# Optimization experiments

Measured on AMD Instinct MI355X. Metric: run time of the kernel, lower is better.

## Reference

```python
import jax, jax.numpy as jnp
import numpy as np

B, T, C = 2, 2048, 768
N_HEADS = 12
HEAD = C // N_HEADS


def setup_inputs() -> dict:
    key = jax.random.key(0)
    k1, k2, k3 = jax.random.split(key, 3)
    x = jax.random.normal(k1, (B, T, C), dtype=jnp.float32)
    # torch Linear weights: [out_features, in_features]
    W_attn = jax.random.normal(k2, (3 * C, C), dtype=jnp.float32) * 0.02
    W_proj = jax.random.normal(k3, (C, C), dtype=jnp.float32) * 0.02
    return {"x": x, "W_attn": W_attn, "W_proj": W_proj}


def reference(x, W_attn, W_proj):
    b, t, c = x.shape
    qkv = jnp.einsum('btc,oc->bto', x, W_attn)  # [B,T,3C]
    q, k, v = jnp.split(qkv, 3, axis=-1)
    # [B, H, T, D]
    q = q.reshape(b, t, N_HEADS, HEAD).transpose(0, 2, 1, 3)
    k = k.reshape(b, t, N_HEADS, HEAD).transpose(0, 2, 1, 3)
    v = v.reshape(b, t, N_HEADS, HEAD).transpose(0, 2, 1, 3)
    scale = 1.0 / jnp.sqrt(jnp.asarray(HEAD, dtype=x.dtype))
    wei = jnp.einsum('bhqd,bhkd->bhqk', q, k) * scale  # [B,H,T,T]
    causal = jnp.tril(jnp.ones((t, t), dtype=bool))
    wei = jnp.where(causal[None, None], wei, jnp.asarray(-jnp.inf, dtype=wei.dtype))
    wei = jax.nn.softmax(wei, axis=-1)  # dropout p=0 -> identity
    out = jnp.einsum('bhqk,bhkd->bhqd', wei, v)
    out = out.transpose(0, 2, 1, 3).reshape(b, t, c)
    out = jnp.einsum('btc,oc->bto', out, W_proj)
    return out
```

## Files before the change

kernel.cpp:

```cpp
#include <hip/hip_runtime.h>

#define T_DIM 2048
#define C_DIM 768
#define NH    12
#define HD    64
#define KDIM  768
#define NJOBS (24 * 32)

typedef __attribute__((ext_vector_type(8))) short short8;
typedef __attribute__((ext_vector_type(4))) float f32x4;
typedef unsigned short u16;

__device__ __forceinline__ u16 f2bf(float f) {
    unsigned int u = __builtin_bit_cast(unsigned int, f);
    u = (u + 0x7fffu + ((u >> 16) & 1u)) >> 16;
    return (u16)u;
}
__device__ __forceinline__ f32x4 max4(f32x4 a, f32x4 b) {
    f32x4 r; r[0]=fmaxf(a[0],b[0]); r[1]=fmaxf(a[1],b[1]);
    r[2]=fmaxf(a[2],b[2]); r[3]=fmaxf(a[3],b[3]); return r;
}
__device__ __forceinline__ unsigned int cvtpk(float a, float b) {
    unsigned int r;
    asm("v_cvt_pk_bf16_f32 %0, %1, %2" : "=v"(r) : "v"(a), "v"(b));
    return r;
}
__device__ __forceinline__ void gload16(const u16* g, u16* l) {
    __builtin_amdgcn_global_load_lds(
        (const __attribute__((address_space(1))) unsigned int*)g,
        (__attribute__((address_space(3))) unsigned int*)l, 16, 0, 0);
}

#define NX  (4096 * 768)
#define NWA (2304 * 768)
#define NWP (768 * 768)
#define TOT4 ((NX + NWA + NWP) / 4)

__global__ __launch_bounds__(256) void convert_all(
    const float* __restrict__ x, const float* __restrict__ wa,
    const float* __restrict__ wp, u16* __restrict__ xb,
    u16* __restrict__ wab, u16* __restrict__ wpb, int* __restrict__ counter)
{
    if (blockIdx.x == 0 && threadIdx.x == 0) *counter = 0;
    for (int i4 = blockIdx.x * 256 + threadIdx.x; i4 < TOT4; i4 += gridDim.x * 256) {
        int i = i4 * 4;
        const float* src; u16* dst; int off;
        if (i < NX)            { src = x;  dst = xb;  off = i; }
        else if (i < NX + NWA) { src = wa; dst = wab; off = i - NX; }
        else                   { src = wp; dst = wpb; off = i - NX - NWA; }
        float4 v = *(const float4*)&src[off];
        ushort4 o;
        o.x = f2bf(v.x); o.y = f2bf(v.y); o.z = f2bf(v.z); o.w = f2bf(v.w);
        *(ushort4*)&dst[off] = o;
    }
}

__global__ __launch_bounds__(256) void gemm_qkv(
    const u16* __restrict__ A, const u16* __restrict__ Wt,
    u16* __restrict__ qb, u16* __restrict__ kb, u16* __restrict__ vtb)
{
    __shared__ __align__(16) u16 AsL[2][128][32];
    __shared__ __align__(16) u16 BsL[2][128][32];

    const int tid = threadIdx.x;
    const int orig = blockIdx.x;
    const int wg = (orig & 7) * 72 + (orig >> 3);
    const int bm = (wg / 18) * 128;
    const int bn = (wg % 18) * 128;

    const int w = tid >> 6, l = tid & 63;
    const int wr = (w >> 1) * 64, wc = (w & 1) * 64;
    const int lrow = l & 15, lg = l >> 4;
    const int lr4 = l >> 2, lc4 = l & 3;

    f32x4 acc[4][4];
    const f32x4 zero4 = {0.f, 0.f, 0.f, 0.f};
#pragma unroll
    for (int mi = 0; mi < 4; ++mi)
#pragma unroll
        for (int ni = 0; ni < 4; ++ni) acc[mi][ni] = zero4;

    auto STAGE = [&](int buf, int k0) {
#pragma unroll
        for (int i = 0; i < 2; ++i) {
            const int rb = w * 32 + i * 16;
            const int row = rb + lr4;
            const int sc = (lc4 ^ (row & 3)) * 8;
            gload16(&A [(size_t)(bm + row) * KDIM + k0 + sc], &AsL[buf][rb][0]);
            gload16(&Wt[(size_t)(bn + row) * KDIM + k0 + sc], &BsL[buf][rb][0]);
        }
    };

    int cur = 0;
    STAGE(0, 0);
    for (int k0 = 0; k0 < KDIM; k0 += 32) {
        __syncthreads();
        if (k0 + 32 < KDIM) STAGE(cur ^ 1, k0 + 32);

        short8 af[4], bf[4];
#pragma unroll
        for (int mi = 0; mi < 4; ++mi)
            af[mi] = *(const short8*)&AsL[cur][wr + mi * 16 + lrow][(lg ^ (lrow & 3)) * 8];
#pragma unroll
        for (int ni = 0; ni < 4; ++ni)
            bf[ni] = *(const short8*)&BsL[cur][wc + ni * 16 + lrow][(lg ^ (lrow & 3)) * 8];
#pragma unroll
        for (int mi = 0; mi < 4; ++mi)
#pragma unroll
            for (int ni = 0; ni < 4; ++ni)
                acc[mi][ni] = __builtin_amdgcn_mfma_f32_16x16x32_bf16(
                    af[mi], bf[ni], acc[mi][ni], 0, 0, 0);
        cur ^= 1;
    }

#pragma unroll
    for (int ni = 0; ni < 4; ++ni) {
        const int colbase = bn + wc + ni * 16;
        const int which = colbase / C_DIM;
        const int h = (colbase % C_DIM) / HD;
        const int d = (colbase % HD) + lrow;
        const float qs = (which == 0) ? 0.125f : 1.0f;
#pragma unroll
        for (int mi = 0; mi < 4; ++mi) {
            const int t0 = bm + wr + mi * 16 + lg * 4;
            const int bb2 = t0 >> 11, tt = t0 & 2047;
            const size_t bhoff = (size_t)(bb2 * NH + h);
            if (which == 2) {
                ushort4 pv;
                pv.x = f2bf(acc[mi][ni][0]); pv.y = f2bf(acc[mi][ni][1]);
                pv.z = f2bf(acc[mi][ni][2]); pv.w = f2bf(acc[mi][ni][3]);
                *(ushort4*)&vtb[(bhoff * HD + d) * T_DIM + tt] = pv;
            } else {
                u16* dst = (which == 0) ? qb : kb;
#pragma unroll
                for (int jj = 0; jj < 4; ++jj)
                    dst[(bhoff * T_DIM + tt + jj) * HD + d] = f2bf(acc[mi][ni][jj] * qs);
            }
        }
    }
}

__global__ __launch_bounds__(256) void gemm_proj(
    const u16* __restrict__ A, const u16* __restrict__ Wt,
    float* __restrict__ dense)
{
    __shared__ __align__(16) u16 As[64][40];
    __shared__ __align__(16) u16 Bs[128][40];

    const int tid = threadIdx.x;
    const int orig = blockIdx.x;
    const int wg = (orig & 7) * 48 + (orig >> 3);
    const int bm = (wg / 6) * 64, bn = (wg % 6) * 128;

    const int w = tid >> 6, l = tid & 63;
    const int wr = (w >> 1) * 32, wc = (w & 1) * 64;
    const int lrow = l & 15, lg = l >> 4;

    const int srow = tid >> 2;
    const int scol = (tid & 3) * 8;

    f32x4 acc[2][4];
    const f32x4 zero4 = {0.f, 0.f, 0.f, 0.f};
#pragma unroll
    for (int mi = 0; mi < 2; ++mi)
#pragma unroll
        for (int ni = 0; ni < 4; ++ni) acc[mi][ni] = zero4;

    uint4 ra0 = *(const uint4*)&A [(size_t)(bm + srow)      * KDIM + scol];
    uint4 rb0 = *(const uint4*)&Wt[(size_t)(bn + srow)      * KDIM + scol];
    uint4 rb1 = *(const uint4*)&Wt[(size_t)(bn + 64 + srow) * KDIM + scol];

    for (int k0 = 0; k0 < KDIM; k0 += 32) {
        __syncthreads();
        *(uint4*)&As[srow][scol]      = ra0;
        *(uint4*)&Bs[srow][scol]      = rb0;
        *(uint4*)&Bs[64 + srow][scol] = rb1;
        __syncthreads();

        if (k0 + 32 < KDIM) {
            ra0 = *(const uint4*)&A [(size_t)(bm + srow)      * KDIM + k0 + 32 + scol];
            rb0 = *(const uint4*)&Wt[(size_t)(bn + srow)      * KDIM + k0 + 32 + scol];
            rb1 = *(const uint4*)&Wt[(size_t)(bn + 64 + srow) * KDIM + k0 + 32 + scol];
        }

        short8 af[2], bf[4];
#pragma unroll
        for (int mi = 0; mi < 2; ++mi)
            af[mi] = *(const short8*)&As[wr + mi * 16 + lrow][lg * 8];
#pragma unroll
        for (int ni = 0; ni < 4; ++ni)
            bf[ni] = *(const short8*)&Bs[wc + ni * 16 + lrow][lg * 8];
#pragma unroll
        for (int mi = 0; mi < 2; ++mi)
#pragma unroll
            for (int ni = 0; ni < 4; ++ni)
                acc[mi][ni] = __builtin_amdgcn_mfma_f32_16x16x32_bf16(
                    af[mi], bf[ni], acc[mi][ni], 0, 0, 0);
    }

#pragma unroll
    for (int ni = 0; ni < 4; ++ni) {
        const int col = bn + wc + ni * 16 + lrow;
#pragma unroll
        for (int mi = 0; mi < 2; ++mi) {
            const int m0 = bm + wr + mi * 16 + lg * 4;
#pragma unroll
            for (int jj = 0; jj < 4; ++jj)
                dense[(size_t)(m0 + jj) * C_DIM + col] = acc[mi][ni][jj];
        }
    }
}

__global__ __launch_bounds__(256, 2) void attn_mfma(
    const u16* __restrict__ q, const u16* __restrict__ k,
    const u16* __restrict__ vt, u16* __restrict__ aw, int* __restrict__ counter)
{
    __shared__ __align__(16) u16 KsL [2][128][64];
    __shared__ __align__(16) u16 VtsL[2][64][128];
    __shared__ __align__(16) u16 Ps  [4][16][72];
    __shared__ int job_s;

    const int tid = threadIdx.x, w = tid >> 6, l = tid & 63;
    const int lrow = l & 15, lg = l >> 4;
    const int lr8 = l >> 3, lc8 = l & 7;
    const int lr16 = l >> 4, lc16 = l & 15;
    const f32x4 zero4 = {0.f, 0.f, 0.f, 0.f};

    for (;;) {
        __syncthreads();
        if (tid == 0) job_s = atomicAdd(counter, 1);
        __syncthreads();
        const int j = job_s;
        if (j >= NJOBS) break;

        const int qt = 31 - (j / 24);
        const int bh = j - (j / 24) * 24;
        const int bb = bh / NH, hh = bh % NH;
        const int qbase = qt * 64 + w * 16;
        const int qg = qbase + lrow;

        const u16* Qp = q  + (size_t)bh * T_DIM * HD;
        const u16* Kp = k  + (size_t)bh * T_DIM * HD;
        const u16* Vp = vt + (size_t)bh * HD * T_DIM;

        const short8 aq0 = *(const short8*)&Qp[(size_t)(qbase + lrow) * HD + lg * 8];
        const short8 aq1 = *(const short8*)&Qp[(size_t)(qbase + lrow) * HD + 32 + lg * 8];

        f32x4 o[4];
#pragma unroll
        for (int n = 0; n < 4; ++n) o[n] = zero4;
        float m_run = -3.0e38f;
        float l_run = 0.0f;

        auto STAGE = [&](int buf, int kk0) {
#pragma unroll
            for (int i = 0; i < 4; ++i) {
                const int rb = w * 32 + i * 8;
                const int row = rb + lr8;
                gload16(&Kp[(size_t)(kk0 + row) * HD + ((lc8 ^ (row & 7)) * 8)],
                        &KsL[buf][rb][0]);
            }
#pragma unroll
            for (int i = 0; i < 4; ++i) {
                const int db = w * 16 + i * 4;
                const int d = db + lr16;
                gload16(&Vp[(size_t)d * T_DIM + kk0 + ((lc16 ^ (d & 15)) * 8)],
                        &VtsL[buf][db][0]);
            }
        };

        auto PROCESS = [&](f32x4* s, int sub, int kk0, bool masked) {
            if (masked) {
#pragma unroll
                for (int n = 0; n < 4; ++n)
#pragma unroll
                    for (int jj = 0; jj < 4; ++jj)
                        if (kk0 + sub * 64 + n * 16 + lg * 4 + jj > qg)
                            s[n][jj] = -3.0e38f;
            }
            f32x4 t2 = max4(max4(s[0], s[1]), max4(s[2], s[3]));
            float rm = fmaxf(fmaxf(t2[0], t2[1]), fmaxf(t2[2], t2[3]));
            rm = fmaxf(rm, __shfl_xor(rm, 16));
            rm = fmaxf(rm, __shfl_xor(rm, 32));
            const float m_new = fmaxf(m_run, rm);
            const float alpha = __expf(m_run - m_new);
            m_run = m_new;
#pragma unroll
            for (int n = 0; n < 4; ++n)
#pragma unroll
                for (int jj = 0; jj < 4; ++jj)
                    s[n][jj] = __expf(s[n][jj] - m_new);
            f32x4 a2 = (s[0] + s[1]) + (s[2] + s[3]);
            float rs = (a2[0] + a2[1]) + (a2[2] + a2[3]);
            rs += __shfl_xor(rs, 16);
            rs += __shfl_xor(rs, 32);
            l_run = l_run * alpha + rs;
#pragma unroll
            for (int n = 0; n < 4; ++n) {
                uint2 pr;
                pr.x = cvtpk(s[n][0], s[n][1]);
                pr.y = cvtpk(s[n][2], s[n][3]);
                *(uint2*)&Ps[w][lrow][n * 16 + lg * 4] = pr;
            }
#pragma unroll
            for (int jj = 0; jj < 4; ++jj) {
                const float aj = __shfl(alpha, lg * 4 + jj);
                o[0][jj] *= aj; o[1][jj] *= aj; o[2][jj] *= aj; o[3][jj] *= aj;
            }
            const short8 ap0 = *(const short8*)&Ps[w][lrow][lg * 8];
            const short8 ap1 = *(const short8*)&Ps[w][lrow][32 + lg * 8];
            const int cur = (kk0 >> 7) & 1;
#pragma unroll
            for (int n = 0; n < 4; ++n) {
                const int row = n * 16 + lrow;
                const short8 bv0 = *(const short8*)
                    &VtsL[cur][row][((sub * 8 + lg) ^ lrow) * 8];
                const short8 bv1 = *(const short8*)
                    &VtsL[cur][row][((sub * 8 + 4 + lg) ^ lrow) * 8];
                o[n] = __builtin_amdgcn_mfma_f32_16x16x32_bf16(ap0, bv0, o[n], 0, 0, 0);
                o[n] = __builtin_amdgcn_mfma_f32_16x16x32_bf16(ap1, bv1, o[n], 0, 0, 0);
            }
        };

        const int nkt = qt / 2 + 1;
        int cur = 0;
        STAGE(0, 0);
        for (int kt = 0; kt < nkt; ++kt) {
            const int kk0 = kt * 128;
            __syncthreads();
            if (kt + 1 < nkt) STAGE(cur ^ 1, kk0 + 128);

            const bool last = (kt == nkt - 1);
            const int nsub = (last && (qt & 1) == 0) ? 1 : 2;

            f32x4 s0[4], s1[4];
#pragma unroll
            for (int n = 0; n < 4; ++n) {
                const int row = n * 16 + lrow;
                const short8 kf0 = *(const short8*)&KsL[cur][row][((lg)     ^ (lrow & 7)) * 8];
                const short8 kf1 = *(const short8*)&KsL[cur][row][((lg + 4) ^ (lrow & 7)) * 8];
                s0[n] = __builtin_amdgcn_mfma_f32_16x16x32_bf16(kf0, aq0, zero4, 0, 0, 0);
                s0[n] = __builtin_amdgcn_mfma_f32_16x16x32_bf16(kf1, aq1, s0[n], 0, 0, 0);
            }
            if (nsub == 2) {
#pragma unroll
                for (int n = 0; n < 4; ++n) {
                    const int row = 64 + n * 16 + lrow;
                    const short8 kf0 = *(const short8*)&KsL[cur][row][((lg)     ^ (lrow & 7)) * 8];
                    const short8 kf1 = *(const short8*)&KsL[cur][row][((lg + 4) ^ (lrow & 7)) * 8];
                    s1[n] = __builtin_amdgcn_mfma_f32_16x16x32_bf16(kf0, aq0, zero4, 0, 0, 0);
                    s1[n] = __builtin_amdgcn_mfma_f32_16x16x32_bf16(kf1, aq1, s1[n], 0, 0, 0);
                }
            }

            PROCESS(s0, 0, kk0, last && nsub == 1);
            if (nsub == 2) PROCESS(s1, 1, kk0, last);

            cur ^= 1;
        }

#pragma unroll
        for (int jj = 0; jj < 4; ++jj) {
            const float lj = __shfl(l_run, lg * 4 + jj);
            const float inv = 1.0f / lj;
            const size_t m = (size_t)bb * T_DIM + qbase + lg * 4 + jj;
#pragma unroll
            for (int n = 0; n < 4; ++n)
                aw[m * C_DIM + hh * HD + n * 16 + lrow] = f2bf(o[n][jj] * inv);
        }
    }
}

extern "C" void kernel_launch(void* const* d_in, const int* in_sizes, int n_in,
                              void* d_out, int out_size, void* d_ws, size_t ws_size,
                              hipStream_t stream) {
    const float* x      = (const float*)d_in[0];
    const float* W_attn = (const float*)d_in[1];
    const float* W_proj = (const float*)d_in[2];
    float* out = (float*)d_out;

    char* ws = (char*)d_ws;
    u16* xb  = (u16*)ws;                       ws += (size_t)NX * 2;
    u16* wab = (u16*)ws;                       ws += (size_t)NWA * 2;
    u16* wpb = (u16*)ws;                       ws += (size_t)NWP * 2;
    u16* qb  = (u16*)ws;                       ws += (size_t)24 * T_DIM * HD * 2;
    u16* kb  = (u16*)ws;                       ws += (size_t)24 * T_DIM * HD * 2;
    u16* vtb = (u16*)ws;                       ws += (size_t)24 * T_DIM * HD * 2;
    u16* awb = (u16*)ws;                       ws += (size_t)4096 * C_DIM * 2;
    int* cnt = (int*)ws;

    convert_all<<<2048, 256, 0, stream>>>(x, W_attn, W_proj, xb, wab, wpb, cnt);

    gemm_qkv<<<576, 256, 0, stream>>>(xb, wab, qb, kb, vtb);

    attn_mfma<<<512, 256, 0, stream>>>(qb, kb, vtb, awb, cnt);

    gemm_proj<<<384, 256, 0, stream>>>(awb, wpb, out);
}
```

Measured before the change: 95.77 us.

## Per-XCD job queues, exp2 softmax with folded log2e, and split online-softmax state

Measured after the change: 99.17 us. +3.5%, slower.

```diff
diff --git a/kernel.cpp b/kernel.cpp
--- a/kernel.cpp
+++ b/kernel.cpp
@@ -5,7 +5,7 @@
 #define NH    12
 #define HD    64
 #define KDIM  768
-#define NJOBS (24 * 32)
+#define JOBS_PER_XCD 96
 
 typedef __attribute__((ext_vector_type(8))) short short8;
 typedef __attribute__((ext_vector_type(4))) float f32x4;
@@ -39,9 +39,9 @@
 __global__ __launch_bounds__(256) void convert_all(
     const float* __restrict__ x, const float* __restrict__ wa,
     const float* __restrict__ wp, u16* __restrict__ xb,
-    u16* __restrict__ wab, u16* __restrict__ wpb, int* __restrict__ counter)
+    u16* __restrict__ wab, u16* __restrict__ wpb, int* __restrict__ counters)
 {
-    if (blockIdx.x == 0 && threadIdx.x == 0) *counter = 0;
+    if (blockIdx.x == 0 && threadIdx.x < 8) counters[threadIdx.x] = 0;
     for (int i4 = blockIdx.x * 256 + threadIdx.x; i4 < TOT4; i4 += gridDim.x * 256) {
         int i = i4 * 4;
         const float* src; u16* dst; int off;
@@ -119,7 +119,7 @@
         const int which = colbase / C_DIM;
         const int h = (colbase % C_DIM) / HD;
         const int d = (colbase % HD) + lrow;
-        const float qs = (which == 0) ? 0.125f : 1.0f;
+        const float qs = (which == 0) ? 0.18033688011112042f : 1.0f;
 #pragma unroll
         for (int mi = 0; mi < 4; ++mi) {
             const int t0 = bm + wr + mi * 16 + lg * 4;
@@ -213,7 +213,7 @@
 
 __global__ __launch_bounds__(256, 2) void attn_mfma(
     const u16* __restrict__ q, const u16* __restrict__ k,
-    const u16* __restrict__ vt, u16* __restrict__ aw, int* __restrict__ counter)
+    const u16* __restrict__ vt, u16* __restrict__ aw, int* __restrict__ counters)
 {
     __shared__ __align__(16) u16 KsL [2][128][64];
     __shared__ __align__(16) u16 VtsL[2][64][128];
@@ -224,17 +224,18 @@
     const int lrow = l & 15, lg = l >> 4;
     const int lr8 = l >> 3, lc8 = l & 7;
     const int lr16 = l >> 4, lc16 = l & 15;
+    const int xcdi = blockIdx.x & 7;
     const f32x4 zero4 = {0.f, 0.f, 0.f, 0.f};
 
     for (;;) {
         __syncthreads();
-        if (tid == 0) job_s = atomicAdd(counter, 1);
+        if (tid == 0) job_s = atomicAdd(&counters[xcdi], 1);
         __syncthreads();
         const int j = job_s;
-        if (j >= NJOBS) break;
-
-        const int qt = 31 - (j / 24);
-        const int bh = j - (j / 24) * 24;
+        if (j >= JOBS_PER_XCD) break;
+
+        const int qt = 31 - (j / 3);
+        const int bh = xcdi * 3 + (j - (j / 3) * 3);
         const int bb = bh / NH, hh = bh % NH;
         const int qbase = qt * 64 + w * 16;
         const int qg = qbase + lrow;
@@ -246,11 +247,11 @@
         const short8 aq0 = *(const short8*)&Qp[(size_t)(qbase + lrow) * HD + lg * 8];
         const short8 aq1 = *(const short8*)&Qp[(size_t)(qbase + lrow) * HD + 32 + lg * 8];
 
-        f32x4 o[4];
-#pragma unroll
-        for (int n = 0; n < 4; ++n) o[n] = zero4;
-        float m_run = -3.0e38f;
-        float l_run = 0.0f;
+        f32x4 o0[4], o1[4];
+#pragma unroll
+        for (int n = 0; n < 4; ++n) { o0[n] = zero4; o1[n] = zero4; }
+        float m0 = -3.0e38f, l0 = 0.0f;
+        float m1 = -3.0e38f, l1 = 0.0f;
 
         auto STAGE = [&](int buf, int kk0) {
 #pragma unroll
@@ -269,7 +270,8 @@
             }
         };
 
-        auto PROCESS = [&](f32x4* s, int sub, int kk0, bool masked) {
+        auto PROCESS = [&](f32x4* s, int sub, int kk0, bool masked,
+                           float& mr, float& lr_, f32x4* oo) {
             if (masked) {
 #pragma unroll
                 for (int n = 0; n < 4; ++n)
@@ -282,19 +284,19 @@
             float rm = fmaxf(fmaxf(t2[0], t2[1]), fmaxf(t2[2], t2[3]));
             rm = fmaxf(rm, __shfl_xor(rm, 16));
             rm = fmaxf(rm, __shfl_xor(rm, 32));
-            const float m_new = fmaxf(m_run, rm);
-            const float alpha = __expf(m_run - m_new);
-            m_run = m_new;
+            const float m_new = fmaxf(mr, rm);
+            const float alpha = exp2f(mr - m_new);
+            mr = m_new;
 #pragma unroll
             for (int n = 0; n < 4; ++n)
 #pragma unroll
                 for (int jj = 0; jj < 4; ++jj)
-                    s[n][jj] = __expf(s[n][jj] - m_new);
+                    s[n][jj] = exp2f(s[n][jj] - m_new);
             f32x4 a2 = (s[0] + s[1]) + (s[2] + s[3]);
             float rs = (a2[0] + a2[1]) + (a2[2] + a2[3]);
             rs += __shfl_xor(rs, 16);
             rs += __shfl_xor(rs, 32);
-            l_run = l_run * alpha + rs;
+            lr_ = lr_ * alpha + rs;
 #pragma unroll
             for (int n = 0; n < 4; ++n) {
                 uint2 pr;
@@ -305,7 +307,7 @@
 #pragma unroll
             for (int jj = 0; jj < 4; ++jj) {
                 const float aj = __shfl(alpha, lg * 4 + jj);
-                o[0][jj] *= aj; o[1][jj] *= aj; o[2][jj] *= aj; o[3][jj] *= aj;
+                oo[0][jj] *= aj; oo[1][jj] *= aj; oo[2][jj] *= aj; oo[3][jj] *= aj;
             }
             const short8 ap0 = *(const short8*)&Ps[w][lrow][lg * 8];
             const short8 ap1 = *(const short8*)&Ps[w][lrow][32 + lg * 8];
@@ -317,8 +319,8 @@
                     &VtsL[cur][row][((sub * 8 + lg) ^ lrow) * 8];
                 const short8 bv1 = *(const short8*)
                     &VtsL[cur][row][((sub * 8 + 4 + lg) ^ lrow) * 8];
-                o[n] = __builtin_amdgcn_mfma_f32_16x16x32_bf16(ap0, bv0, o[n], 0, 0, 0);
-                o[n] = __builtin_amdgcn_mfma_f32_16x16x32_bf16(ap1, bv1, o[n], 0, 0, 0);
+                oo[n] = __builtin_amdgcn_mfma_f32_16x16x32_bf16(ap0, bv0, oo[n], 0, 0, 0);
+                oo[n] = __builtin_amdgcn_mfma_f32_16x16x32_bf16(ap1, bv1, oo[n], 0, 0, 0);
             }
         };
 
@@ -353,20 +355,27 @@
                 }
             }
 
-            PROCESS(s0, 0, kk0, last && nsub == 1);
-            if (nsub == 2) PROCESS(s1, 1, kk0, last);
+            PROCESS(s0, 0, kk0, last && nsub == 1, m0, l0, o0);
+            if (nsub == 2) PROCESS(s1, 1, kk0, last, m1, l1, o1);
 
             cur ^= 1;
         }
 
+        const float mf = fmaxf(m0, m1);
+        const float a0 = exp2f(m0 - mf);
+        const float a1 = exp2f(m1 - mf);
+        const float inv = 1.0f / (l0 * a0 + l1 * a1);
 #pragma unroll
         for (int jj = 0; jj < 4; ++jj) {
-            const float lj = __shfl(l_run, lg * 4 + jj);
-            const float inv = 1.0f / lj;
-            const size_t m = (size_t)bb * T_DIM + qbase + lg * 4 + jj;
+            const int qrow = lg * 4 + jj;
+            const float a0j = __shfl(a0, qrow);
+            const float a1j = __shfl(a1, qrow);
+            const float invj = __shfl(inv, qrow);
+            const size_t m = (size_t)bb * T_DIM + qbase + qrow;
 #pragma unroll
             for (int n = 0; n < 4; ++n)
-                aw[m * C_DIM + hh * HD + n * 16 + lrow] = f2bf(o[n][jj] * inv);
+                aw[m * C_DIM + hh * HD + n * 16 + lrow] =
+                    f2bf((o0[n][jj] * a0j + o1[n][jj] * a1j) * invj);
         }
     }
 }
```
